# Optimization experiments

Measured on AMD Instinct MI355X. Metric: run time of the kernel, lower is better.

Reference implementation:

```python
import jax, jax.numpy as jnp
import numpy as np

NH = 8  # n_heads

def ln(x, g, b, eps=1e-5):
    m = x.mean(-1, keepdims=True)
    v = ((x - m) ** 2).mean(-1, keepdims=True)
    return (x - m) / jnp.sqrt(v + eps) * g + b

def setup_inputs() -> dict:
    key0 = jax.random.key(0)
    ks = jax.random.split(key0, 16)
    B, C, F, H = 4, 8, 2048, 512
    Hf = 2 * H
    s = 0.02
    return {
        'query': jax.random.normal(ks[0], (B, F, H), jnp.float32),
        'key': jax.random.normal(ks[1], (B, C, F, H), jnp.float32),
        'value': jax.random.normal(ks[2], (B, C, F, H), jnp.float32),
        'Wq': jax.random.normal(ks[3], (H, H), jnp.float32) * s,
        'bq': jnp.zeros((H,), jnp.float32),
        'Wk': jax.random.normal(ks[4], (H, H), jnp.float32) * s,
        'bk': jnp.zeros((H,), jnp.float32),
        'Wv': jax.random.normal(ks[5], (H, H), jnp.float32) * s,
        'bv': jnp.zeros((H,), jnp.float32),
        'Wo': jax.random.normal(ks[6], (H, H), jnp.float32) * s,
        'bo': jnp.zeros((H,), jnp.float32),
        'ln1_g': jnp.ones((H,), jnp.float32),
        'ln1_b': jnp.zeros((H,), jnp.float32),
        'W1': jax.random.normal(ks[7], (Hf, H), jnp.float32) * s,
        'b1': jnp.zeros((Hf,), jnp.float32),
        'W2': jax.random.normal(ks[8], (H, Hf), jnp.float32) * s,
        'b2': jnp.zeros((H,), jnp.float32),
        'ln2_g': jnp.ones((H,), jnp.float32),
        'ln2_b': jnp.zeros((H,), jnp.float32),
    }

def reference(query, key, value, Wq, bq, Wk, bk, Wv, bv, Wo, bo,
              ln1_g, ln1_b, W1, b1, W2, b2, ln2_g, ln2_b):
    B0, F0, H = query.shape
    # faithful to the original torch reshapes (pure reinterpretation, not permute)
    q = query.reshape(F0, B0, 1, H)                                   # [F,B,1,H]
    k = key.reshape(key.shape[2], key.shape[0], key.shape[1], key.shape[3])    # [F,B,C,H]
    v = value.reshape(value.shape[2], value.shape[0], value.shape[1], value.shape[3])
    dh = H // NH
    def heads(x):
        f, b, s, _ = x.shape
        return x.reshape(f, b, s, NH, dh).transpose(0, 1, 3, 2, 4)    # [F,B,nh,S,dh]
    Q = heads(q @ Wq.T + bq)
    K = heads(k @ Wk.T + bk)
    V = heads(v @ Wv.T + bv)
    scale = jnp.sqrt(jnp.float32(dh))
    att = jax.nn.softmax(jnp.einsum('fbhqd,fbhkd->fbhqk', Q, K) / scale, axis=-1)
    x = jnp.einsum('fbhqk,fbhkd->fbhqd', att, V)                      # [F,B,nh,1,dh]
    x = x.transpose(0, 1, 3, 2, 4).reshape(F0, B0, -1, H)
    x = x @ Wo.T + bo
    h1 = ln(q + x, ln1_g, ln1_b)                                      # residual + LN
    ff = jax.nn.relu(h1 @ W1.T + b1) @ W2.T + b2                      # FFN (dropout=eval identity)
    out = ln(h1 + ff, ln2_g, ln2_b)                                   # [F,B,1,H]
    return out.reshape(B0, F0, H)
```

## Files before the change

kernel.cpp:

```cpp
#include <hip/hip_runtime.h>
#include <cstdint>
#include <cstddef>

#define DEVFN static __device__ __forceinline__

typedef __attribute__((ext_vector_type(4))) float f32x4;
typedef __attribute__((ext_vector_type(8))) __bf16 bf16x8;

typedef __attribute__((address_space(1))) void gvoid;
typedef __attribute__((address_space(3))) void svoid;

DEVFN unsigned short f32_to_bf16_bits(float f) {
  uint32_t u = __builtin_bit_cast(uint32_t, f);
  return (unsigned short)((u + 0x7fffu + ((u >> 16) & 1u)) >> 16);
}
DEVFN float bf16_lo(uint32_t d) { return __builtin_bit_cast(float, d << 16); }
DEVFN float bf16_hi(uint32_t d) { return __builtin_bit_cast(float, d & 0xffff0000u); }
DEVFN uint32_t pack_bf16x2(float lo, float hi) {
  return (uint32_t)f32_to_bf16_bits(lo) | ((uint32_t)f32_to_bf16_bits(hi) << 16);
}

DEVFN void load_lds16(const void* g, void* l) {
  __builtin_amdgcn_global_load_lds((const gvoid*)g, (svoid*)l, 16, 0, 0);
}

__global__ __launch_bounds__(256) void cvt_all(
    const float* __restrict__ q, const float* __restrict__ Wq,
    const float* __restrict__ Wv, const float* __restrict__ Wo,
    const float* __restrict__ W1, const float* __restrict__ W2,
    const float* __restrict__ Wk,
    unsigned short* __restrict__ qb, unsigned short* __restrict__ Wqb,
    unsigned short* __restrict__ Wvb, unsigned short* __restrict__ Wob,
    unsigned short* __restrict__ W1b, unsigned short* __restrict__ W2b,
    unsigned short* __restrict__ WkT) {
  int i = (int)(blockIdx.x * 256 + threadIdx.x);
  if (i >= 753664) {
    int off = i - 753664;
    int oidx = off * 8;
    int d0 = oidx & 63;
    int j = (oidx >> 6) & 511;
    int h = oidx >> 15;
    union { unsigned short s[8]; uint4 v; } o;
#pragma unroll
    for (int t = 0; t < 8; ++t)
      o.s[t] = f32_to_bf16_bits(Wk[(size_t)((h << 6) + d0 + t) * 512 + j]);
    ((uint4*)WkT)[off] = o.v;
    return;
  }
  const float* src;
  unsigned short* dst;
  int off;
  if (i < 524288)      { src = q;  dst = qb;  off = i; }
  else if (i < 557056) { src = Wq; dst = Wqb; off = i - 524288; }
  else if (i < 589824) { src = Wv; dst = Wvb; off = i - 557056; }
  else if (i < 622592) { src = Wo; dst = Wob; off = i - 589824; }
  else if (i < 688128) { src = W1; dst = W1b; off = i - 622592; }
  else                 { src = W2; dst = W2b; off = i - 688128; }
  const float4* p = (const float4*)src;
  float4 a = p[2 * off], b = p[2 * off + 1];
  union { unsigned short s[8]; uint4 v; } o;
  o.s[0] = f32_to_bf16_bits(a.x); o.s[1] = f32_to_bf16_bits(a.y);
  o.s[2] = f32_to_bf16_bits(a.z); o.s[3] = f32_to_bf16_bits(a.w);
  o.s[4] = f32_to_bf16_bits(b.x); o.s[5] = f32_to_bf16_bits(b.y);
  o.s[6] = f32_to_bf16_bits(b.z); o.s[7] = f32_to_bf16_bits(b.w);
  ((uint4*)dst)[off] = o.v;
}

template<int BM, int BN, bool OUT_BF16, bool RELU, bool ADD_RES>
__global__ __launch_bounds__(256)
void gemm_bt(const unsigned short* __restrict__ A, int lda, long long zA,
             const unsigned short* __restrict__ Bt, int ldb, long long zB,
             void* __restrict__ Cv, int ldc, long long zC,
             const float* __restrict__ bias, int zBias,
             const float* __restrict__ res, int ldres,
             int K) {
  constexpr int MT = BM / 32;
  constexpr int NT = BN / 32;
  constexpr int AQ = BM / 64;
  constexpr int BQ = BN / 64;
  __shared__ __align__(16) unsigned short As[BM * 32];
  __shared__ __align__(16) unsigned short Bs[BN * 32];

  const int tid = (int)threadIdx.x;
  const int lane = tid & 63;
  const int w = tid >> 6;
  const int wm = w >> 1;
  const int wn = w & 1;
  const int m0 = (int)blockIdx.y * BM;
  const int n0 = (int)blockIdx.x * BN;
  const long long z = (long long)blockIdx.z;

  A += z * zA;
  Bt += z * zB;
  const float* biasz = bias ? (bias + z * zBias) : nullptr;

  f32x4 acc[MT][NT];
#pragma unroll
  for (int i = 0; i < MT; ++i)
#pragma unroll
    for (int j = 0; j < NT; ++j) acc[i][j] = f32x4{0.f, 0.f, 0.f, 0.f};

  int rA[AQ], cA[AQ], rB[BQ], cB[BQ];
#pragma unroll
  for (int q = 0; q < AQ; ++q) {
    const int o = q * 4096 + w * 1024 + lane * 16;
    rA[q] = o >> 6; cA[q] = (o & 63) >> 1;
  }
#pragma unroll
  for (int q = 0; q < BQ; ++q) {
    const int o = q * 4096 + w * 1024 + lane * 16;
    rB[q] = o >> 6; cB[q] = (o & 63) >> 1;
  }

  const int kIters = K / 32;
  for (int kt = 0; kt < kIters; ++kt) {
    const int k0 = kt * 32;
    __syncthreads();
#pragma unroll
    for (int q = 0; q < AQ; ++q)
      load_lds16(A + (size_t)(m0 + rA[q]) * lda + (k0 + cA[q]), As + q * 2048 + w * 512);
#pragma unroll
    for (int q = 0; q < BQ; ++q)
      load_lds16(Bt + (size_t)(n0 + rB[q]) * ldb + (k0 + cB[q]), Bs + q * 2048 + w * 512);
    asm volatile("s_waitcnt vmcnt(0)" ::: "memory");
    __syncthreads();

    const int fr = lane & 15;
    const int kq = lane >> 4;
    bf16x8 af[MT], bf[NT];
#pragma unroll
    for (int i = 0; i < MT; ++i) {
      const int m = wm * (BM / 2) + i * 16 + fr;
      af[i] = __builtin_bit_cast(bf16x8, *(const uint4*)(As + m * 32 + kq * 8));
    }
#pragma unroll
    for (int j = 0; j < NT; ++j) {
      const int n = wn * (BN / 2) + j * 16 + fr;
      bf[j] = __builtin_bit_cast(bf16x8, *(const uint4*)(Bs + n * 32 + kq * 8));
    }
#pragma unroll
    for (int i = 0; i < MT; ++i)
#pragma unroll
      for (int j = 0; j < NT; ++j)
        acc[i][j] = __builtin_amdgcn_mfma_f32_16x16x32_bf16(af[i], bf[j], acc[i][j], 0, 0, 0);
  }

  const int fr = lane & 15;
  const int rq = lane >> 4;
  unsigned short* Cb = (unsigned short*)Cv + z * zC;
  float* Cf = (float*)Cv + z * zC;
#pragma unroll
  for (int i = 0; i < MT; ++i) {
    const int rbase = m0 + wm * (BM / 2) + i * 16 + rq * 4;
#pragma unroll
    for (int j = 0; j < NT; ++j) {
      const int col = n0 + wn * (BN / 2) + j * 16 + fr;
      const float bvv = biasz ? biasz[col] : 0.f;
#pragma unroll
      for (int r = 0; r < 4; ++r) {
        float v = acc[i][j][r] + bvv;
        if (ADD_RES) v += res[(size_t)(rbase + r) * ldres + col];
        if (RELU) v = fmaxf(v, 0.f);
        if (OUT_BF16) Cb[(size_t)(rbase + r) * ldc + col] = f32_to_bf16_bits(v);
        else Cf[(size_t)(rbase + r) * ldc + col] = v;
      }
    }
  }
}

__global__ __launch_bounds__(256) void attn_kernel(const float* __restrict__ key,
                                                   const float* __restrict__ value,
                                                   unsigned short* __restrict__ U) {
  const int lane = (int)threadIdx.x & 63;
  const int n = (int)blockIdx.x * 4 + ((int)threadIdx.x >> 6);

  const uint4* Uq = (const uint4*)(U + (size_t)n * 4096);
  float u[8][8];
#pragma unroll
  for (int h = 0; h < 8; ++h) {
    uint4 d = Uq[h * 64 + lane];
    u[h][0] = bf16_lo(d.x); u[h][1] = bf16_hi(d.x);
    u[h][2] = bf16_lo(d.y); u[h][3] = bf16_hi(d.y);
    u[h][4] = bf16_lo(d.z); u[h][5] = bf16_hi(d.z);
    u[h][6] = bf16_lo(d.w); u[h][7] = bf16_hi(d.w);
  }

  float zc[8][8];
#pragma unroll
  for (int c = 0; c < 8; ++c) {
    const float4* kp = (const float4*)(key + ((size_t)n * 8 + c) * 512);
    float4 k0 = kp[lane * 2];
    float4 k1 = kp[lane * 2 + 1];
    float p[8];
#pragma unroll
    for (int h = 0; h < 8; ++h) {
      p[h] = u[h][0] * k0.x + u[h][1] * k0.y + u[h][2] * k0.z + u[h][3] * k0.w +
             u[h][4] * k1.x + u[h][5] * k1.y + u[h][6] * k1.z + u[h][7] * k1.w;
    }
#pragma unroll
    for (int off = 1; off < 64; off <<= 1) {
#pragma unroll
      for (int h = 0; h < 8; ++h) p[h] += __shfl_xor(p[h], off, 64);
    }
#pragma unroll
    for (int h = 0; h < 8; ++h) zc[h][c] = p[h] * 0.125f;
  }

#pragma unroll
  for (int h = 0; h < 8; ++h) {
    float m = zc[h][0];
#pragma unroll
    for (int c = 1; c < 8; ++c) m = fmaxf(m, zc[h][c]);
    float se = 0.f;
#pragma unroll
    for (int c = 0; c < 8; ++c) { zc[h][c] = __expf(zc[h][c] - m); se += zc[h][c]; }
    const float inv = 1.f / se;
#pragma unroll
    for (int c = 0; c < 8; ++c) zc[h][c] *= inv;
  }

  float acc[8][8];
#pragma unroll
  for (int h = 0; h < 8; ++h)
#pragma unroll
    for (int t = 0; t < 8; ++t) acc[h][t] = 0.f;
#pragma unroll
  for (int c = 0; c < 8; ++c) {
    const float4* vp = (const float4*)(value + ((size_t)n * 8 + c) * 512);
    float4 v0 = vp[lane * 2];
    float4 v1 = vp[lane * 2 + 1];
#pragma unroll
    for (int h = 0; h < 8; ++h) {
      const float a = zc[h][c];
      acc[h][0] += a * v0.x; acc[h][1] += a * v0.y;
      acc[h][2] += a * v0.z; acc[h][3] += a * v0.w;
      acc[h][4] += a * v1.x; acc[h][5] += a * v1.y;
      acc[h][6] += a * v1.z; acc[h][7] += a * v1.w;
    }
  }

  uint4* Uw = (uint4*)(U + (size_t)n * 4096);
#pragma unroll
  for (int h = 0; h < 8; ++h) {
    uint4 o;
    o.x = pack_bf16x2(acc[h][0], acc[h][1]);
    o.y = pack_bf16x2(acc[h][2], acc[h][3]);
    o.z = pack_bf16x2(acc[h][4], acc[h][5]);
    o.w = pack_bf16x2(acc[h][6], acc[h][7]);
    Uw[h * 64 + lane] = o;
  }
}

__global__ __launch_bounds__(256) void ln_kernel(const float* __restrict__ in,
                                                 const float* __restrict__ g,
                                                 const float* __restrict__ b,
                                                 float* __restrict__ outf,
                                                 unsigned short* __restrict__ outb) {
  const int lane = (int)threadIdx.x & 63;
  const size_t row = (size_t)blockIdx.x * 4 + (threadIdx.x >> 6);
  const int col = lane * 8;
  const float* x = in + row * 512;
  float4 a0 = *(const float4*)(x + col);
  float4 a1 = *(const float4*)(x + col + 4);
  float v[8] = {a0.x, a0.y, a0.z, a0.w, a1.x, a1.y, a1.z, a1.w};
  float s = 0.f, sq = 0.f;
#pragma unroll
  for (int t = 0; t < 8; ++t) { s += v[t]; sq += v[t] * v[t]; }
#pragma unroll
  for (int off = 32; off > 0; off >>= 1) {
    s += __shfl_xor(s, off, 64);
    sq += __shfl_xor(sq, off, 64);
  }
  const float mean = s * (1.f / 512.f);
  const float var = sq * (1.f / 512.f) - mean * mean;
  const float rstd = rsqrtf(var + 1e-5f);
  float o[8];
#pragma unroll
  for (int t = 0; t < 8; ++t) o[t] = (v[t] - mean) * rstd * g[col + t] + b[col + t];
  if (outf) {
    *(float4*)(outf + row * 512 + col) = make_float4(o[0], o[1], o[2], o[3]);
    *(float4*)(outf + row * 512 + col + 4) = make_float4(o[4], o[5], o[6], o[7]);
  }
  if (outb) {
    union { unsigned short s_[8]; uint4 v_; } u;
#pragma unroll
    for (int t = 0; t < 8; ++t) u.s_[t] = f32_to_bf16_bits(o[t]);
    *(uint4*)(outb + row * 512 + col) = u.v_;
  }
}

extern "C" void kernel_launch(void* const* d_in, const int* in_sizes, int n_in,
                              void* d_out, int out_size, void* d_ws, size_t ws_size,
                              hipStream_t stream) {
  const float* query = (const float*)d_in[0];
  const float* key   = (const float*)d_in[1];
  const float* value = (const float*)d_in[2];
  const float* Wq = (const float*)d_in[3];
  const float* bq = (const float*)d_in[4];
  const float* Wk = (const float*)d_in[5];
  const float* Wv = (const float*)d_in[7];
  const float* bv = (const float*)d_in[8];
  const float* Wo = (const float*)d_in[9];
  const float* bo = (const float*)d_in[10];
  const float* ln1g = (const float*)d_in[11];
  const float* ln1b = (const float*)d_in[12];
  const float* W1 = (const float*)d_in[13];
  const float* b1 = (const float*)d_in[14];
  const float* W2 = (const float*)d_in[15];
  const float* b2 = (const float*)d_in[16];
  const float* ln2g = (const float*)d_in[17];
  const float* ln2b = (const float*)d_in[18];
  float* out = (float*)d_out;

  char* ws = (char*)d_ws;
  size_t off = 0;
  auto alloc = [&](size_t bytes) -> void* {
    off = (off + 255) & ~(size_t)255;
    void* p = ws + off;
    off += bytes;
    return p;
  };

  const int N = 8192;
  unsigned short* qb   = (unsigned short*)alloc((size_t)N * 512 * 2);
  unsigned short* Wqb  = (unsigned short*)alloc(512 * 512 * 2);
  unsigned short* Wvb  = (unsigned short*)alloc(512 * 512 * 2);
  unsigned short* Wob  = (unsigned short*)alloc(512 * 512 * 2);
  unsigned short* W1b  = (unsigned short*)alloc(1024 * 512 * 2);
  unsigned short* W2b  = (unsigned short*)alloc(512 * 1024 * 2);
  unsigned short* WkT  = (unsigned short*)alloc(8 * 512 * 64 * 2);
  unsigned short* Qp   = (unsigned short*)alloc((size_t)N * 512 * 2);
  unsigned short* U    = (unsigned short*)alloc((size_t)N * 4096 * 2);
  float*          h1pre= (float*)alloc((size_t)N * 512 * 4);
  unsigned short* h1b  = (unsigned short*)alloc((size_t)N * 512 * 2);
  float*          h1f  = (float*)alloc((size_t)N * 512 * 4);
  unsigned short* mid  = (unsigned short*)alloc((size_t)N * 1024 * 2);
  unsigned short* x    = Qp;
  float*          o2pre= h1pre;
  (void)ws_size; (void)in_sizes; (void)n_in; (void)out_size;

  dim3 blk(256);
  cvt_all<<<3072, blk, 0, stream>>>(query, Wq, Wv, Wo, W1, W2, Wk,
                                    qb, Wqb, Wvb, Wob, W1b, W2b, WkT);

  gemm_bt<64, 64, true, false, false><<<dim3(8, 128, 1), blk, 0, stream>>>(
      qb, 512, 0, Wqb, 512, 0, Qp, 512, 0, bq, 0, nullptr, 0, 512);
  gemm_bt<128, 128, true, false, false><<<dim3(4, 64, 8), blk, 0, stream>>>(
      Qp, 512, 64, WkT, 64, 32768, U, 4096, 512, nullptr, 0, nullptr, 0, 64);
  attn_kernel<<<2048, blk, 0, stream>>>(key, value, U);
  gemm_bt<64, 64, true, false, false><<<dim3(1, 128, 8), blk, 0, stream>>>(
      U, 4096, 512, Wvb, 512, 32768, x, 512, 64, bv, 64, nullptr, 0, 512);
  gemm_bt<64, 64, false, false, true><<<dim3(8, 128, 1), blk, 0, stream>>>(
      x, 512, 0, Wob, 512, 0, h1pre, 512, 0, bo, 0, query, 512, 512);
  ln_kernel<<<2048, blk, 0, stream>>>(h1pre, ln1g, ln1b, h1f, h1b);
  gemm_bt<64, 64, true, true, false><<<dim3(16, 128, 1), blk, 0, stream>>>(
      h1b, 512, 0, W1b, 512, 0, mid, 1024, 0, b1, 0, nullptr, 0, 512);
  gemm_bt<64, 64, false, false, true><<<dim3(8, 128, 1), blk, 0, stream>>>(
      mid, 1024, 0, W2b, 1024, 0, o2pre, 512, 0, b2, 0, h1f, 512, 1024);
  ln_kernel<<<2048, blk, 0, stream>>>(o2pre, ln2g, ln2b, out, nullptr);
}
```

Baseline: 509.3 us.

## Stage attention key/value/U via async LDS loads and enlarge GEMM tiles

The attention kernel now runs one wave per block and issues async global-to-LDS loads for key, U and value up front. It waits only for key and U before the score computation, so value loads overlap the softmax work. The per-lane column mapping is changed to interleaved 4-element chunks, consistently for reads and writes. Several projection and FFN GEMMs switch from 64x64 to 128x128 tiles. The 40KB of LDS per single-wave block may limit occupancy, and larger tiles reduce grid size.

Measured after the change: 521.4 us. +2.4%, slower.

```diff
diff --git a/kernel.cpp b/kernel.cpp
--- a/kernel.cpp
+++ b/kernel.cpp
@@ -168,29 +168,45 @@
   }
 }
 
-__global__ __launch_bounds__(256) void attn_kernel(const float* __restrict__ key,
-                                                   const float* __restrict__ value,
-                                                   unsigned short* __restrict__ U) {
-  const int lane = (int)threadIdx.x & 63;
-  const int n = (int)blockIdx.x * 4 + ((int)threadIdx.x >> 6);
-
-  const uint4* Uq = (const uint4*)(U + (size_t)n * 4096);
+__global__ __launch_bounds__(64) void attn_kernel(const float* __restrict__ key,
+                                                  const float* __restrict__ value,
+                                                  unsigned short* __restrict__ U) {
+  __shared__ __align__(16) float kls[4096];
+  __shared__ __align__(16) float vls[4096];
+  __shared__ __align__(16) unsigned short uls[4096];
+  const int lane = (int)threadIdx.x;
+  const int n = (int)blockIdx.x;
+
+  const float* kg = key + (size_t)n * 4096 + lane * 4;
+  const float* vg = value + (size_t)n * 4096 + lane * 4;
+  const unsigned short* ug = U + (size_t)n * 4096 + lane * 8;
+
+#pragma unroll
+  for (int j = 0; j < 16; ++j) load_lds16(kg + j * 256, kls + j * 256);
+#pragma unroll
+  for (int j = 0; j < 8; ++j) load_lds16(ug + j * 512, uls + j * 512);
+#pragma unroll
+  for (int j = 0; j < 16; ++j) load_lds16(vg + j * 256, vls + j * 256);
+
+  asm volatile("s_waitcnt vmcnt(16)" ::: "memory");
+  __builtin_amdgcn_sched_barrier(0);
+
   float u[8][8];
 #pragma unroll
   for (int h = 0; h < 8; ++h) {
-    uint4 d = Uq[h * 64 + lane];
-    u[h][0] = bf16_lo(d.x); u[h][1] = bf16_hi(d.x);
-    u[h][2] = bf16_lo(d.y); u[h][3] = bf16_hi(d.y);
-    u[h][4] = bf16_lo(d.z); u[h][5] = bf16_hi(d.z);
-    u[h][6] = bf16_lo(d.w); u[h][7] = bf16_hi(d.w);
+    uint2 a = *(const uint2*)(uls + h * 512 + 4 * lane);
+    uint2 b = *(const uint2*)(uls + h * 512 + 256 + 4 * lane);
+    u[h][0] = bf16_lo(a.x); u[h][1] = bf16_hi(a.x);
+    u[h][2] = bf16_lo(a.y); u[h][3] = bf16_hi(a.y);
+    u[h][4] = bf16_lo(b.x); u[h][5] = bf16_hi(b.x);
+    u[h][6] = bf16_lo(b.y); u[h][7] = bf16_hi(b.y);
   }
 
   float zc[8][8];
 #pragma unroll
   for (int c = 0; c < 8; ++c) {
-    const float4* kp = (const float4*)(key + ((size_t)n * 8 + c) * 512);
-    float4 k0 = kp[lane * 2];
-    float4 k1 = kp[lane * 2 + 1];
+    const float4 k0 = *(const float4*)(kls + c * 512 + 4 * lane);
+    const float4 k1 = *(const float4*)(kls + c * 512 + 256 + 4 * lane);
     float p[8];
 #pragma unroll
     for (int h = 0; h < 8; ++h) {
@@ -219,6 +235,9 @@
     for (int c = 0; c < 8; ++c) zc[h][c] *= inv;
   }
 
+  asm volatile("s_waitcnt vmcnt(0)" ::: "memory");
+  __builtin_amdgcn_sched_barrier(0);
+
   float acc[8][8];
 #pragma unroll
   for (int h = 0; h < 8; ++h)
@@ -226,9 +245,8 @@
     for (int t = 0; t < 8; ++t) acc[h][t] = 0.f;
 #pragma unroll
   for (int c = 0; c < 8; ++c) {
-    const float4* vp = (const float4*)(value + ((size_t)n * 8 + c) * 512);
-    float4 v0 = vp[lane * 2];
-    float4 v1 = vp[lane * 2 + 1];
+    const float4 v0 = *(const float4*)(vls + c * 512 + 4 * lane);
+    const float4 v1 = *(const float4*)(vls + c * 512 + 256 + 4 * lane);
 #pragma unroll
     for (int h = 0; h < 8; ++h) {
       const float a = zc[h][c];
@@ -239,15 +257,16 @@
     }
   }
 
-  uint4* Uw = (uint4*)(U + (size_t)n * 4096);
+  unsigned short* Uw = U + (size_t)n * 4096;
 #pragma unroll
   for (int h = 0; h < 8; ++h) {
-    uint4 o;
-    o.x = pack_bf16x2(acc[h][0], acc[h][1]);
-    o.y = pack_bf16x2(acc[h][2], acc[h][3]);
-    o.z = pack_bf16x2(acc[h][4], acc[h][5]);
-    o.w = pack_bf16x2(acc[h][6], acc[h][7]);
-    Uw[h * 64 + lane] = o;
+    uint2 oA, oB;
+    oA.x = pack_bf16x2(acc[h][0], acc[h][1]);
+    oA.y = pack_bf16x2(acc[h][2], acc[h][3]);
+    oB.x = pack_bf16x2(acc[h][4], acc[h][5]);
+    oB.y = pack_bf16x2(acc[h][6], acc[h][7]);
+    *(uint2*)(Uw + h * 512 + 4 * lane) = oA;
+    *(uint2*)(Uw + h * 512 + 256 + 4 * lane) = oB;
   }
 }
 
@@ -343,19 +362,19 @@
   cvt_all<<<3072, blk, 0, stream>>>(query, Wq, Wv, Wo, W1, W2, Wk,
                                     qb, Wqb, Wvb, Wob, W1b, W2b, WkT);
 
-  gemm_bt<64, 64, true, false, false><<<dim3(8, 128, 1), blk, 0, stream>>>(
+  gemm_bt<128, 128, true, false, false><<<dim3(4, 64, 1), blk, 0, stream>>>(
       qb, 512, 0, Wqb, 512, 0, Qp, 512, 0, bq, 0, nullptr, 0, 512);
   gemm_bt<128, 128, true, false, false><<<dim3(4, 64, 8), blk, 0, stream>>>(
       Qp, 512, 64, WkT, 64, 32768, U, 4096, 512, nullptr, 0, nullptr, 0, 64);
-  attn_kernel<<<2048, blk, 0, stream>>>(key, value, U);
+  attn_kernel<<<8192, dim3(64), 0, stream>>>(key, value, U);
   gemm_bt<64, 64, true, false, false><<<dim3(1, 128, 8), blk, 0, stream>>>(
       U, 4096, 512, Wvb, 512, 32768, x, 512, 64, bv, 64, nullptr, 0, 512);
-  gemm_bt<64, 64, false, false, true><<<dim3(8, 128, 1), blk, 0, stream>>>(
+  gemm_bt<128, 128, false, false, true><<<dim3(4, 64, 1), blk, 0, stream>>>(
       x, 512, 0, Wob, 512, 0, h1pre, 512, 0, bo, 0, query, 512, 512);
   ln_kernel<<<2048, blk, 0, stream>>>(h1pre, ln1g, ln1b, h1f, h1b);
-  gemm_bt<64, 64, true, true, false><<<dim3(16, 128, 1), blk, 0, stream>>>(
+  gemm_bt<128, 128, true, true, false><<<dim3(8, 64, 1), blk, 0, stream>>>(
       h1b, 512, 0, W1b, 512, 0, mid, 1024, 0, b1, 0, nullptr, 0, 512);
-  gemm_bt<64, 64, false, false, true><<<dim3(8, 128, 1), blk, 0, stream>>>(
+  gemm_bt<128, 128, false, false, true><<<dim3(4, 64, 1), blk, 0, stream>>>(
       mid, 1024, 0, W2b, 1024, 0, o2pre, 512, 0, b2, 0, h1f, 512, 1024);
   ln_kernel<<<2048, blk, 0, stream>>>(o2pre, ln2g, ln2b, out, nullptr);
 }
```

## Compute attention scores with bf16 MFMA and share probabilities via LDS

Applied to the files above, without the earlier changes.

The attention kernel now has each wavefront handle two tokens. The 8 heads by 8 contexts scores come from a single 16x16x32 bf16 MFMA chain over the 512-wide dimension, with the next operands prefetched each step. This replaces per-head dot products followed by 64-lane shuffle reductions. Softmax uses short 8-lane shuffles, the probabilities are staged in LDS, and the value accumulation then stays scalar FMA with coalesced loads. Keys are rounded to bf16 for the scores, which lowers precision, and the grid is halved with launch bounds set for occupancy.

Result: no change. 500.1 us (-1.8%).

```diff
diff --git a/kernel.cpp b/kernel.cpp
--- a/kernel.cpp
+++ b/kernel.cpp
@@ -168,86 +168,97 @@
   }
 }
 
-__global__ __launch_bounds__(256) void attn_kernel(const float* __restrict__ key,
-                                                   const float* __restrict__ value,
-                                                   unsigned short* __restrict__ U) {
+__global__ __launch_bounds__(256, 4) void attn_kernel(const float* __restrict__ key,
+                                                      const float* __restrict__ value,
+                                                      unsigned short* __restrict__ U) {
+  __shared__ float att_lds[4][128];
   const int lane = (int)threadIdx.x & 63;
-  const int n = (int)blockIdx.x * 4 + ((int)threadIdx.x >> 6);
-
-  const uint4* Uq = (const uint4*)(U + (size_t)n * 4096);
-  float u[8][8];
-#pragma unroll
-  for (int h = 0; h < 8; ++h) {
-    uint4 d = Uq[h * 64 + lane];
-    u[h][0] = bf16_lo(d.x); u[h][1] = bf16_hi(d.x);
-    u[h][2] = bf16_lo(d.y); u[h][3] = bf16_hi(d.y);
-    u[h][4] = bf16_lo(d.z); u[h][5] = bf16_hi(d.z);
-    u[h][6] = bf16_lo(d.w); u[h][7] = bf16_hi(d.w);
-  }
-
-  float zc[8][8];
-#pragma unroll
-  for (int c = 0; c < 8; ++c) {
-    const float4* kp = (const float4*)(key + ((size_t)n * 8 + c) * 512);
-    float4 k0 = kp[lane * 2];
-    float4 k1 = kp[lane * 2 + 1];
-    float p[8];
+  const int w = (int)threadIdx.x >> 6;
+  const int n0 = (int)blockIdx.x * 8 + w * 2;
+  const int fr = lane & 15;
+  const int kq = lane >> 4;
+  const int tok = fr >> 3;
+  const int hc = fr & 7;
+
+  const unsigned short* Ap = U + (size_t)(n0 + tok) * 4096 + hc * 512 + kq * 8;
+  const float* Kp = key + ((size_t)(n0 + tok) * 8 + hc) * 512 + kq * 8;
+
+  f32x4 sc = f32x4{0.f, 0.f, 0.f, 0.f};
+  uint4 aC = *(const uint4*)Ap;
+  float4 k0C = *(const float4*)Kp;
+  float4 k1C = *(const float4*)(Kp + 4);
+#pragma unroll
+  for (int kt = 0; kt < 16; ++kt) {
+    uint4 aN = aC;
+    float4 k0N = k0C, k1N = k1C;
+    if (kt + 1 < 16) {
+      aN = *(const uint4*)(Ap + (kt + 1) * 32);
+      k0N = *(const float4*)(Kp + (kt + 1) * 32);
+      k1N = *(const float4*)(Kp + (kt + 1) * 32 + 4);
+    }
+    union { uint32_t u[4]; bf16x8 v; } bk;
+    bk.u[0] = pack_bf16x2(k0C.x, k0C.y);
+    bk.u[1] = pack_bf16x2(k0C.z, k0C.w);
+    bk.u[2] = pack_bf16x2(k1C.x, k1C.y);
+    bk.u[3] = pack_bf16x2(k1C.z, k1C.w);
+    sc = __builtin_amdgcn_mfma_f32_16x16x32_bf16(
+        __builtin_bit_cast(bf16x8, aC), bk.v, sc, 0, 0, 0);
+    aC = aN; k0C = k0N; k1C = k1N;
+  }
+
+  float av[4];
+#pragma unroll
+  for (int r = 0; r < 4; ++r) {
+    const float v = sc[r] * 0.125f;
+    float m = v;
+#pragma unroll
+    for (int off = 1; off < 8; off <<= 1) m = fmaxf(m, __shfl_xor(m, off, 64));
+    const float e = __expf(v - m);
+    float s = e;
+#pragma unroll
+    for (int off = 1; off < 8; off <<= 1) s += __shfl_xor(s, off, 64);
+    av[r] = e / s;
+  }
+
+  if ((kq >> 1) == (fr >> 3)) {
+    *(float4*)&att_lds[w][(fr >> 3) * 64 + (fr & 7) * 8 + (kq & 1) * 4] =
+        make_float4(av[0], av[1], av[2], av[3]);
+  }
+
+#pragma unroll
+  for (int t = 0; t < 2; ++t) {
+    const float* vbase = value + (size_t)(n0 + t) * 4096;
+    float acc[8][8];
+#pragma unroll
+    for (int h = 0; h < 8; ++h)
+#pragma unroll
+      for (int e = 0; e < 8; ++e) acc[h][e] = 0.f;
+#pragma unroll
+    for (int c = 0; c < 8; ++c) {
+      const float4 v0 = *(const float4*)(vbase + c * 512 + 4 * lane);
+      const float4 v1 = *(const float4*)(vbase + c * 512 + 256 + 4 * lane);
+      const float4 a0 = *(const float4*)&att_lds[w][t * 64 + c * 8 + 0];
+      const float4 a1 = *(const float4*)&att_lds[w][t * 64 + c * 8 + 4];
+      const float ah[8] = {a0.x, a0.y, a0.z, a0.w, a1.x, a1.y, a1.z, a1.w};
+#pragma unroll
+      for (int h = 0; h < 8; ++h) {
+        acc[h][0] += ah[h] * v0.x; acc[h][1] += ah[h] * v0.y;
+        acc[h][2] += ah[h] * v0.z; acc[h][3] += ah[h] * v0.w;
+        acc[h][4] += ah[h] * v1.x; acc[h][5] += ah[h] * v1.y;
+        acc[h][6] += ah[h] * v1.z; acc[h][7] += ah[h] * v1.w;
+      }
+    }
+    unsigned short* Uw = U + (size_t)(n0 + t) * 4096;
 #pragma unroll
     for (int h = 0; h < 8; ++h) {
-      p[h] = u[h][0] * k0.x + u[h][1] * k0.y + u[h][2] * k0.z + u[h][3] * k0.w +
-             u[h][4] * k1.x + u[h][5] * k1.y + u[h][6] * k1.z + u[h][7] * k1.w;
-    }
-#pragma unroll
-    for (int off = 1; off < 64; off <<= 1) {
-#pragma unroll
-      for (int h = 0; h < 8; ++h) p[h] += __shfl_xor(p[h], off, 64);
-    }
-#pragma unroll
-    for (int h = 0; h < 8; ++h) zc[h][c] = p[h] * 0.125f;
-  }
-
-#pragma unroll
-  for (int h = 0; h < 8; ++h) {
-    float m = zc[h][0];
-#pragma unroll
-    for (int c = 1; c < 8; ++c) m = fmaxf(m, zc[h][c]);
-    float se = 0.f;
-#pragma unroll
-    for (int c = 0; c < 8; ++c) { zc[h][c] = __expf(zc[h][c] - m); se += zc[h][c]; }
-    const float inv = 1.f / se;
-#pragma unroll
-    for (int c = 0; c < 8; ++c) zc[h][c] *= inv;
-  }
-
-  float acc[8][8];
-#pragma unroll
-  for (int h = 0; h < 8; ++h)
-#pragma unroll
-    for (int t = 0; t < 8; ++t) acc[h][t] = 0.f;
-#pragma unroll
-  for (int c = 0; c < 8; ++c) {
-    const float4* vp = (const float4*)(value + ((size_t)n * 8 + c) * 512);
-    float4 v0 = vp[lane * 2];
-    float4 v1 = vp[lane * 2 + 1];
-#pragma unroll
-    for (int h = 0; h < 8; ++h) {
-      const float a = zc[h][c];
-      acc[h][0] += a * v0.x; acc[h][1] += a * v0.y;
-      acc[h][2] += a * v0.z; acc[h][3] += a * v0.w;
-      acc[h][4] += a * v1.x; acc[h][5] += a * v1.y;
-      acc[h][6] += a * v1.z; acc[h][7] += a * v1.w;
-    }
-  }
-
-  uint4* Uw = (uint4*)(U + (size_t)n * 4096);
-#pragma unroll
-  for (int h = 0; h < 8; ++h) {
-    uint4 o;
-    o.x = pack_bf16x2(acc[h][0], acc[h][1]);
-    o.y = pack_bf16x2(acc[h][2], acc[h][3]);
-    o.z = pack_bf16x2(acc[h][4], acc[h][5]);
-    o.w = pack_bf16x2(acc[h][6], acc[h][7]);
-    Uw[h * 64 + lane] = o;
+      uint2 oA, oB;
+      oA.x = pack_bf16x2(acc[h][0], acc[h][1]);
+      oA.y = pack_bf16x2(acc[h][2], acc[h][3]);
+      oB.x = pack_bf16x2(acc[h][4], acc[h][5]);
+      oB.y = pack_bf16x2(acc[h][6], acc[h][7]);
+      *(uint2*)(Uw + h * 512 + 4 * lane) = oA;
+      *(uint2*)(Uw + h * 512 + 256 + 4 * lane) = oB;
+    }
   }
 }
 
@@ -347,7 +358,7 @@
       qb, 512, 0, Wqb, 512, 0, Qp, 512, 0, bq, 0, nullptr, 0, 512);
   gemm_bt<128, 128, true, false, false><<<dim3(4, 64, 8), blk, 0, stream>>>(
       Qp, 512, 64, WkT, 64, 32768, U, 4096, 512, nullptr, 0, nullptr, 0, 64);
-  attn_kernel<<<2048, blk, 0, stream>>>(key, value, U);
+  attn_kernel<<<1024, blk, 0, stream>>>(key, value, U);
   gemm_bt<64, 64, true, false, false><<<dim3(1, 128, 8), blk, 0, stream>>>(
       U, 4096, 512, Wvb, 512, 32768, x, 512, 64, bv, 64, nullptr, 0, 512);
   gemm_bt<64, 64, false, false, true><<<dim3(8, 128, 1), blk, 0, stream>>>(
```
